# Optimization experiments

Measured on AMD Instinct MI355X. Metric: run time of the kernel, lower is better.

Reference implementation:

```python
import jax, jax.numpy as jnp
import numpy as np
from jax import lax

NUM_CLASSES = 80
RADIUS = 2.5
TOPK = 10
IOU_W = 3.0
CLS_W = 1.0
A = 33600
G = 256
IMG = 640.0


def setup_inputs() -> dict:
    key = jax.random.key(0)
    k1, k2, k3, k4, k5, k6, k7 = jax.random.split(key, 7)

    def _boxes(kc, kw, n):
        c = jax.random.uniform(kc, (n, 2), jnp.float32, 0.0, IMG)
        wh = jax.random.uniform(kw, (n, 2), jnp.float32, 8.0, 128.0)
        return jnp.concatenate([c - wh / 2, c + wh / 2], axis=1)

    return {
        "pred_scores": jax.random.normal(k1, (A, NUM_CLASSES), jnp.float32),
        "pred_bboxes": _boxes(k2, k3, A),
        "anchor_points": jax.random.uniform(k6, (A, 2), jnp.float32, 0.0, IMG),
        "gt_labels": jax.random.randint(k7, (G,), 0, NUM_CLASSES),
        "gt_bboxes": _boxes(k4, k5, G),
    }


def _inside_flags(anchor_points, gt_bboxes):
    # [G, A] bool: anchor inside GT box AND inside center-sampling region
    ax = anchor_points[None, :, 0]  # [1, A]
    ay = anchor_points[None, :, 1]
    x1, y1, x2, y2 = (gt_bboxes[:, i:i + 1] for i in range(4))  # each [G, 1]
    in_gt = (ax >= x1) & (ax <= x2) & (ay >= y1) & (ay <= y2)
    cx, cy = (x1 + x2) / 2, (y1 + y2) / 2
    rx, ry = RADIUS * (x2 - x1), RADIUS * (y2 - y1)
    in_center = (ax >= cx - rx) & (ax <= cx + rx) & (ay >= cy - ry) & (ay <= cy + ry)
    return in_gt & in_center


def _pairwise_iou(gt_bboxes, pred_bboxes, eps=1e-6):
    # [G, A]
    lt = jnp.maximum(gt_bboxes[:, None, :2], pred_bboxes[None, :, :2])
    rb = jnp.minimum(gt_bboxes[:, None, 2:], pred_bboxes[None, :, 2:])
    wh = jnp.clip(rb - lt, 0.0)
    overlap = wh[..., 0] * wh[..., 1]
    area_g = (gt_bboxes[:, 2] - gt_bboxes[:, 0]) * (gt_bboxes[:, 3] - gt_bboxes[:, 1])
    area_p = (pred_bboxes[:, 2] - pred_bboxes[:, 0]) * (pred_bboxes[:, 3] - pred_bboxes[:, 1])
    union = area_g[:, None] + area_p[None, :] - overlap + eps
    return overlap / union


def _simota(pred_scores, pred_bboxes, anchor_points, gt_labels, gt_bboxes):
    num_gt = gt_bboxes.shape[0]
    num_anchors = pred_scores.shape[0]
    gt_labels = gt_labels.astype(jnp.int32)

    inside = _inside_flags(anchor_points, gt_bboxes)  # [G, A] bool
    ious = _pairwise_iou(gt_bboxes, pred_bboxes)      # [G, A]

    # BCE(sigmoid(s), one_hot(l)) summed over classes, without [G, A, C]:
    # cost[g,a] = -sum_c log(1-p[a,c]) - (log p[a,l_g] - log(1-p[a,l_g]))
    logp = jax.nn.log_sigmoid(pred_scores)       # [A, C] = log p
    log1mp = jax.nn.log_sigmoid(-pred_scores)    # [A, C] = log(1-p)
    cls_cost = -(logp - log1mp)[:, gt_labels].T - log1mp.sum(-1)[None, :]  # [G, A]

    iou_cost = -jnp.log(ious)
    cost = CLS_W * cls_cost + IOU_W * iou_cost + (~inside).astype(cost_dtype := jnp.float32) * 1e10
    cost = lax.stop_gradient(cost)  # cost only feeds integer top-k indices

    num_candidates = ((ious * inside.astype(ious.dtype)) > 0).sum(axis=1)
    dynamic_ks = jnp.clip(num_candidates, 1, TOPK)  # [G]

    # fixed top-TOPK smallest cost per GT, mask to dynamic_k
    _, topk_idx = lax.top_k(-cost, TOPK)  # [G, TOPK]
    valid = jnp.arange(TOPK)[None, :] < dynamic_ks[:, None]
    idx = jnp.where(valid, topk_idx, num_anchors)  # invalid -> sentinel slot
    g_ids = jnp.broadcast_to(jnp.arange(num_gt, dtype=jnp.int32)[:, None], (num_gt, TOPK))
    # sequential overwrite by ascending gt index == per-anchor max gt index
    assigned = (jnp.full((num_anchors + 1,), -1, jnp.int32)
                .at[idx.reshape(-1)].max(g_ids.reshape(-1)))[:num_anchors]

    pos = assigned >= 0
    safe_g = jnp.where(pos, assigned, 0)
    assigned_labels = jnp.where(pos, gt_labels[safe_g], NUM_CLASSES)
    assigned_bboxes = jnp.where(pos[:, None], gt_bboxes[safe_g], 0.0)
    pos_iou = ious[safe_g, jnp.arange(num_anchors)]
    assigned_scores = (jnp.zeros((num_anchors, NUM_CLASSES + 1), ious.dtype)
                       .at[jnp.arange(num_anchors), assigned_labels]
                       .set(jnp.where(pos, pos_iou, 0.0)))
    return assigned_labels, assigned_bboxes, assigned_scores


def reference(pred_scores, pred_bboxes, anchor_points, gt_labels, gt_bboxes):
    return _simota(pred_scores, pred_bboxes, anchor_points, gt_labels, gt_bboxes)
```

## Files before the change

### kernel.cpp

```cpp
#include <hip/hip_runtime.h>
#include <climits>

#define A_N 33600
#define G_N 256
#define NC 80
#define KK 10
#define CAP 2048
#define NLOAD 8
#define GCHUNK 32
#define NCHUNK (G_N / GCHUNK)
#define FBSEG 16
#define FBSEG_LEN (A_N / FBSEG)
#define INIT_BLKS (A_N / 4)
#define FB_BLKS (G_N * FBSEG)

__device__ __forceinline__ unsigned int ford(float f) {
    unsigned int u = __float_as_uint(f);
    return (u & 0x80000000u) ? ~u : (u | 0x80000000u);
}

__device__ __forceinline__ unsigned long long umin64(unsigned long long a, unsigned long long b) {
    return a < b ? a : b;
}

__global__ __launch_bounds__(256) void k_init(
    const float* __restrict__ scores, const float* __restrict__ pred_b,
    const float* __restrict__ gt_b,
    float* __restrict__ logsum, int* __restrict__ cnt, int* __restrict__ assigned,
    int* __restrict__ fbseg,
    float* __restrict__ out_labels, float4* __restrict__ out_bbox4,
    float4* __restrict__ out_scores4)
{
    int b = blockIdx.x, tid = threadIdx.x;
    int lane = tid & 63, wid = tid >> 6;

    if (b >= INIT_BLKS) {
        int idx = b - INIT_BLKS;
        int g = idx >> 4, seg = idx & (FBSEG - 1);
        __shared__ int smin[4];
        float4 gb = ((const float4*)gt_b)[g];
        int best = INT_MAX;
        int a0 = seg * FBSEG_LEN;
        for (int a = a0 + tid; a < a0 + FBSEG_LEN; a += 256) {
            float4 pb = ((const float4*)pred_b)[a];
            float w = fminf(gb.z, pb.z) - fmaxf(gb.x, pb.x);
            float h = fminf(gb.w, pb.w) - fmaxf(gb.y, pb.y);
            if (w > 0.f && h > 0.f && a < best) best = a;
        }
        #pragma unroll
        for (int off = 32; off; off >>= 1) best = min(best, __shfl_down(best, off));
        if (lane == 0) smin[wid] = best;
        __syncthreads();
        if (tid == 0)
            fbseg[g * FBSEG + seg] = min(min(smin[0], smin[1]), min(smin[2], smin[3]));
        return;
    }

    int t = b * 256 + tid;
    float4 z4 = make_float4(0.f, 0.f, 0.f, 0.f);
    if (t < G_N) cnt[t] = 0;
    if (t < A_N) { assigned[t] = -1; out_labels[t] = (float)NC; out_bbox4[t] = z4; }
    if (t < (A_N * 81) / 4) out_scores4[t] = z4;

    int wv = t >> 6;
    const float* row = scores + (long)wv * NC;
    float acc = 0.f;
    for (int c = lane; c < NC; c += 64) {
        float s = row[c];
        acc -= (fmaxf(s, 0.f) + log1pf(expf(-fabsf(s))));
    }
    #pragma unroll
    for (int off = 32; off > 0; off >>= 1) acc += __shfl_down(acc, off);
    if (lane == 0) logsum[wv] = acc;
}

__global__ __launch_bounds__(256) void k_pairs(
    const float* __restrict__ scores, const float* __restrict__ pred_b,
    const float* __restrict__ anchors, const int* __restrict__ gt_labels,
    const float* __restrict__ gt_b, const float* __restrict__ logsum,
    unsigned long long* __restrict__ bucket, int* __restrict__ cnt)
{
    __shared__ float4 gbox[GCHUNK];
    __shared__ int glab[GCHUNK];
    int tid = threadIdx.x;
    int gc = blockIdx.y;
    if (tid < GCHUNK) {
        gbox[tid] = ((const float4*)gt_b)[gc * GCHUNK + tid];
        glab[tid] = gt_labels[gc * GCHUNK + tid];
    }
    __syncthreads();

    int a = blockIdx.x * 256 + tid;
    if (a >= A_N) return;

    float4 pb = ((const float4*)pred_b)[a];
    float2 ap = ((const float2*)anchors)[a];
    float area_p = (pb.z - pb.x) * (pb.w - pb.y);
    float ls = logsum[a];

    #pragma unroll 4
    for (int g = 0; g < GCHUNK; g++) {
        float4 gb = gbox[g];
        bool in_gt = (ap.x >= gb.x) & (ap.x <= gb.z) & (ap.y >= gb.y) & (ap.y <= gb.w);
        if (!in_gt) continue;

        float ltx = fmaxf(gb.x, pb.x), lty = fmaxf(gb.y, pb.y);
        float rbx = fminf(gb.z, pb.z), rby = fminf(gb.w, pb.w);
        float w = fmaxf(rbx - ltx, 0.f), h = fmaxf(rby - lty, 0.f);
        float overlap = w * h;
        if (!(overlap > 0.f)) continue;

        int gg = gc * GCHUNK + g;
        float area_g = (gb.z - gb.x) * (gb.w - gb.y);
        float uni = area_g + area_p - overlap + 1e-6f;
        float iou = overlap / uni;
        float s = scores[(long)a * NC + glab[g]];
        float cost = (-s - ls) + 3.0f * (-logf(iou));
        unsigned long long key = ((unsigned long long)ford(cost) << 32) | (unsigned)a;

        int slot = atomicAdd(&cnt[gg], 1);
        if (slot < CAP) bucket[(size_t)gg * CAP + slot] = key;
    }
}

__global__ __launch_bounds__(256) void k_select(
    const unsigned long long* __restrict__ bucket, const int* __restrict__ cnt_arr,
    const int* __restrict__ fbseg, int* __restrict__ assigned, int* __restrict__ poslist)
{
    int g = blockIdx.x, tid = threadIdx.x;
    int wid = tid >> 6, lane = tid & 63;
    __shared__ unsigned long long swin[4];
    __shared__ unsigned long long sel[KK];

    int cnt = cnt_arr[g];

    if (cnt == 0) {
        int v = (tid < FBSEG) ? fbseg[g * FBSEG + tid] : INT_MAX;
        if (tid < 64) {
            #pragma unroll
            for (int off = 8; off; off >>= 1) v = min(v, __shfl_down(v, off));
        }
        if (tid == 0) {
            if (v == INT_MAX) v = 0;
            atomicMax(&assigned[v], g);
            poslist[g * KK] = v;
            #pragma unroll
            for (int i = 1; i < KK; i++) poslist[g * KK + i] = -1;
        }
        return;
    }

    int k = cnt < KK ? cnt : KK;
    int nreal = cnt < CAP ? cnt : CAP;
    const unsigned long long* bk = bucket + (size_t)g * CAP;
    unsigned long long kv[NLOAD];
    #pragma unroll
    for (int i = 0; i < NLOAD; i++) {
        int idx = tid + i * 256;
        kv[i] = (idx < nreal) ? bk[idx] : ~0ull;
    }

    for (int it = 0; it < k; it++) {
        unsigned long long m = kv[0];
        #pragma unroll
        for (int i = 1; i < NLOAD; i++) m = umin64(m, kv[i]);
        #pragma unroll
        for (int off = 32; off; off >>= 1) m = umin64(m, __shfl_down(m, off));
        if (lane == 0) swin[wid] = m;
        __syncthreads();
        if (tid == 0)
            sel[it] = umin64(umin64(swin[0], swin[1]), umin64(swin[2], swin[3]));
        __syncthreads();
        unsigned long long win = sel[it];
        #pragma unroll
        for (int i = 0; i < NLOAD; i++) if (kv[i] == win) kv[i] = ~0ull;
    }

    if (tid < KK) poslist[g * KK + tid] = (tid < k) ? (int)(sel[tid] & 0xffffffffu) : -1;
    if (tid < k) atomicMax(&assigned[(int)(sel[tid] & 0xffffffffu)], g);
}

__global__ __launch_bounds__(256) void k_fix(
    const int* __restrict__ poslist, const int* __restrict__ assigned,
    const int* __restrict__ gt_labels, const float* __restrict__ gt_b,
    const float* __restrict__ pred_b,
    float* __restrict__ out_labels, float4* __restrict__ out_bbox4,
    float* __restrict__ out_scores)
{
    int t = blockIdx.x * 256 + threadIdx.x;
    if (t >= G_N * KK) return;
    int a = poslist[t];
    if (a < 0) return;
    int g = assigned[a];
    int label = gt_labels[g];
    float4 gb = ((const float4*)gt_b)[g];
    float4 pb = ((const float4*)pred_b)[a];
    float w = fminf(gb.z, pb.z) - fmaxf(gb.x, pb.x);
    float h = fminf(gb.w, pb.w) - fmaxf(gb.y, pb.y);
    float ovl = fmaxf(w, 0.f) * fmaxf(h, 0.f);
    float area_g = (gb.z - gb.x) * (gb.w - gb.y);
    float area_p = (pb.z - pb.x) * (pb.w - pb.y);
    float uni = area_g + area_p - ovl + 1e-6f;
    float iou = ovl / uni;
    out_labels[a] = (float)label;
    out_bbox4[a] = gb;
    out_scores[(long)a * (NC + 1) + label] = iou;
}

extern "C" void kernel_launch(void* const* d_in, const int* in_sizes, int n_in,
                              void* d_out, int out_size, void* d_ws, size_t ws_size,
                              hipStream_t stream) {
    const float* pred_scores   = (const float*)d_in[0];
    const float* pred_bboxes   = (const float*)d_in[1];
    const float* anchor_points = (const float*)d_in[2];
    const int*   gt_labels     = (const int*)d_in[3];
    const float* gt_bboxes     = (const float*)d_in[4];

    char* ws = (char*)d_ws;
    unsigned long long* bucket = (unsigned long long*)ws;
    size_t off = (size_t)G_N * CAP * 8;
    int*   assigned = (int*)(ws + off);   off += (size_t)A_N * 4;
    int*   cnt      = (int*)(ws + off);   off += (size_t)G_N * 4;
    int*   fbseg    = (int*)(ws + off);   off += (size_t)G_N * FBSEG * 4;
    int*   poslist  = (int*)(ws + off);   off += (size_t)G_N * KK * 4;
    float* logsum   = (float*)(ws + off);

    float*  out_labels = (float*)d_out;
    float4* out_bbox4  = (float4*)(out_labels + A_N);
    float*  out_scores = out_labels + 5 * (size_t)A_N;

    k_init<<<INIT_BLKS + FB_BLKS, 256, 0, stream>>>(
        pred_scores, pred_bboxes, gt_bboxes, logsum, cnt, assigned, fbseg,
        out_labels, out_bbox4, (float4*)out_scores);
    dim3 pg((A_N + 255) / 256, NCHUNK);
    k_pairs<<<pg, 256, 0, stream>>>(pred_scores, pred_bboxes, anchor_points,
                                    gt_labels, gt_bboxes, logsum, bucket, cnt);
    k_select<<<G_N, 256, 0, stream>>>(bucket, cnt, fbseg, assigned, poslist);
    k_fix<<<(G_N * KK + 255) / 256, 256, 0, stream>>>(poslist, assigned, gt_labels,
                                                      gt_bboxes, pred_bboxes,
                                                      out_labels, out_bbox4, out_scores);
}
```

Measured before the change: 45.39 us.

## Fuse init and pair kernels, recompute logsum inline, single-wave select

The init kernel and the pair-cost kernel become one launch. The BCE log-sum is computed per anchor inside each pair block, replacing the precomputed logsum buffer. The eager per-GT fallback scan over all anchors is replaced by a lazy wave-level early-exit scan inside k_select, which runs only when a GT has no candidates. k_select now uses one 64-lane wave with 32 registers per lane, so its reductions need no shared memory or block barriers, and cnt is zeroed by hipMemsetAsync. The cost is that the transcendental logsum work is repeated for each of the 8 GT chunks, and every thread reads a full strided score row.

```diff
diff --git a/kernel.cpp b/kernel.cpp
--- a/kernel.cpp
+++ b/kernel.cpp
@@ -6,13 +6,13 @@
 #define NC 80
 #define KK 10
 #define CAP 2048
-#define NLOAD 8
 #define GCHUNK 32
 #define NCHUNK (G_N / GCHUNK)
-#define FBSEG 16
-#define FBSEG_LEN (A_N / FBSEG)
-#define INIT_BLKS (A_N / 4)
-#define FB_BLKS (G_N * FBSEG)
+#define AB_N 132
+#define PAIR_BLKS (AB_N * NCHUNK)
+#define FILL_N ((A_N * 81) / 4)
+#define FILL_BLKS ((FILL_N + 255) / 256)
+#define NLD 32
 
 __device__ __forceinline__ unsigned int ford(float f) {
     unsigned int u = __float_as_uint(f);
@@ -23,80 +23,52 @@
     return a < b ? a : b;
 }
 
-__global__ __launch_bounds__(256) void k_init(
+__global__ __launch_bounds__(256) void k_main(
     const float* __restrict__ scores, const float* __restrict__ pred_b,
+    const float* __restrict__ anchors, const int* __restrict__ gt_labels,
     const float* __restrict__ gt_b,
-    float* __restrict__ logsum, int* __restrict__ cnt, int* __restrict__ assigned,
-    int* __restrict__ fbseg,
+    unsigned long long* __restrict__ bucket, int* __restrict__ cnt,
+    int* __restrict__ assigned,
     float* __restrict__ out_labels, float4* __restrict__ out_bbox4,
     float4* __restrict__ out_scores4)
 {
-    int b = blockIdx.x, tid = threadIdx.x;
-    int lane = tid & 63, wid = tid >> 6;
-
-    if (b >= INIT_BLKS) {
-        int idx = b - INIT_BLKS;
-        int g = idx >> 4, seg = idx & (FBSEG - 1);
-        __shared__ int smin[4];
-        float4 gb = ((const float4*)gt_b)[g];
-        int best = INT_MAX;
-        int a0 = seg * FBSEG_LEN;
-        for (int a = a0 + tid; a < a0 + FBSEG_LEN; a += 256) {
-            float4 pb = ((const float4*)pred_b)[a];
-            float w = fminf(gb.z, pb.z) - fmaxf(gb.x, pb.x);
-            float h = fminf(gb.w, pb.w) - fmaxf(gb.y, pb.y);
-            if (w > 0.f && h > 0.f && a < best) best = a;
-        }
-        #pragma unroll
-        for (int off = 32; off; off >>= 1) best = min(best, __shfl_down(best, off));
-        if (lane == 0) smin[wid] = best;
-        __syncthreads();
-        if (tid == 0)
-            fbseg[g * FBSEG + seg] = min(min(smin[0], smin[1]), min(smin[2], smin[3]));
+    int bid = blockIdx.x, tid = threadIdx.x;
+
+    if (bid >= PAIR_BLKS) {
+        int t = (bid - PAIR_BLKS) * 256 + tid;
+        float4 z4 = make_float4(0.f, 0.f, 0.f, 0.f);
+        if (t < A_N) { assigned[t] = -1; out_labels[t] = (float)NC; out_bbox4[t] = z4; }
+        if (t < FILL_N) out_scores4[t] = z4;
         return;
     }
 
-    int t = b * 256 + tid;
-    float4 z4 = make_float4(0.f, 0.f, 0.f, 0.f);
-    if (t < G_N) cnt[t] = 0;
-    if (t < A_N) { assigned[t] = -1; out_labels[t] = (float)NC; out_bbox4[t] = z4; }
-    if (t < (A_N * 81) / 4) out_scores4[t] = z4;
-
-    int wv = t >> 6;
-    const float* row = scores + (long)wv * NC;
-    float acc = 0.f;
-    for (int c = lane; c < NC; c += 64) {
-        float s = row[c];
-        acc -= (fmaxf(s, 0.f) + log1pf(expf(-fabsf(s))));
-    }
-    #pragma unroll
-    for (int off = 32; off > 0; off >>= 1) acc += __shfl_down(acc, off);
-    if (lane == 0) logsum[wv] = acc;
-}
-
-__global__ __launch_bounds__(256) void k_pairs(
-    const float* __restrict__ scores, const float* __restrict__ pred_b,
-    const float* __restrict__ anchors, const int* __restrict__ gt_labels,
-    const float* __restrict__ gt_b, const float* __restrict__ logsum,
-    unsigned long long* __restrict__ bucket, int* __restrict__ cnt)
-{
     __shared__ float4 gbox[GCHUNK];
     __shared__ int glab[GCHUNK];
-    int tid = threadIdx.x;
-    int gc = blockIdx.y;
+    int gc = bid & (NCHUNK - 1);
+    int ab = bid >> 3;
     if (tid < GCHUNK) {
         gbox[tid] = ((const float4*)gt_b)[gc * GCHUNK + tid];
         glab[tid] = gt_labels[gc * GCHUNK + tid];
     }
     __syncthreads();
 
-    int a = blockIdx.x * 256 + tid;
+    int a = ab * 256 + tid;
     if (a >= A_N) return;
 
     float4 pb = ((const float4*)pred_b)[a];
     float2 ap = ((const float2*)anchors)[a];
     float area_p = (pb.z - pb.x) * (pb.w - pb.y);
-    float ls = logsum[a];
+
+    const float4* row = (const float4*)(scores + (long)a * NC);
+    float ls = 0.f;
+    #pragma unroll 4
+    for (int i = 0; i < NC / 4; i++) {
+        float4 v = row[i];
+        ls -= fmaxf(v.x, 0.f) + log1pf(expf(-fabsf(v.x)));
+        ls -= fmaxf(v.y, 0.f) + log1pf(expf(-fabsf(v.y)));
+        ls -= fmaxf(v.z, 0.f) + log1pf(expf(-fabsf(v.z)));
+        ls -= fmaxf(v.w, 0.f) + log1pf(expf(-fabsf(v.w)));
+    }
 
     #pragma unroll 4
     for (int g = 0; g < GCHUNK; g++) {
@@ -119,65 +91,65 @@
         unsigned long long key = ((unsigned long long)ford(cost) << 32) | (unsigned)a;
 
         int slot = atomicAdd(&cnt[gg], 1);
-        if (slot < CAP) bucket[(size_t)gg * CAP + slot] = key;
-    }
-}
-
-__global__ __launch_bounds__(256) void k_select(
+        if ((unsigned)slot < CAP) bucket[(size_t)gg * CAP + slot] = key;
+    }
+}
+
+__global__ __launch_bounds__(64) void k_select(
     const unsigned long long* __restrict__ bucket, const int* __restrict__ cnt_arr,
-    const int* __restrict__ fbseg, int* __restrict__ assigned, int* __restrict__ poslist)
+    const float* __restrict__ pred_b, const float* __restrict__ gt_b,
+    int* __restrict__ assigned, int* __restrict__ poslist)
 {
-    int g = blockIdx.x, tid = threadIdx.x;
-    int wid = tid >> 6, lane = tid & 63;
-    __shared__ unsigned long long swin[4];
-    __shared__ unsigned long long sel[KK];
-
+    int g = blockIdx.x, lane = threadIdx.x;
     int cnt = cnt_arr[g];
 
     if (cnt == 0) {
-        int v = (tid < FBSEG) ? fbseg[g * FBSEG + tid] : INT_MAX;
-        if (tid < 64) {
-            #pragma unroll
-            for (int off = 8; off; off >>= 1) v = min(v, __shfl_down(v, off));
+        float4 gb = ((const float4*)gt_b)[g];
+        int found = INT_MAX;
+        for (int base = 0; base < A_N; base += 64) {
+            int a = base + lane;
+            float4 pb = ((const float4*)pred_b)[a];
+            float w = fminf(gb.z, pb.z) - fmaxf(gb.x, pb.x);
+            float h = fminf(gb.w, pb.w) - fmaxf(gb.y, pb.y);
+            bool hit = (w > 0.f) && (h > 0.f);
+            if (__ballot(hit)) { if (hit) found = a; break; }
         }
-        if (tid == 0) {
-            if (v == INT_MAX) v = 0;
-            atomicMax(&assigned[v], g);
-            poslist[g * KK] = v;
-            #pragma unroll
-            for (int i = 1; i < KK; i++) poslist[g * KK + i] = -1;
-        }
+        #pragma unroll
+        for (int off = 32; off; off >>= 1) found = min(found, __shfl_xor(found, off));
+        int m = (found == INT_MAX) ? 0 : found;
+        if (lane == 0) atomicMax(&assigned[m], g);
+        if (lane < KK) poslist[g * KK + lane] = (lane == 0) ? m : -1;
         return;
     }
 
     int k = cnt < KK ? cnt : KK;
     int nreal = cnt < CAP ? cnt : CAP;
     const unsigned long long* bk = bucket + (size_t)g * CAP;
-    unsigned long long kv[NLOAD];
+
+    unsigned long long kv[NLD];
     #pragma unroll
-    for (int i = 0; i < NLOAD; i++) {
-        int idx = tid + i * 256;
-        kv[i] = (idx < nreal) ? bk[idx] : ~0ull;
-    }
-
+    for (int i = 0; i < NLD; i++) {
+        kv[i] = ~0ull;
+        if (i * 64 < nreal) {
+            int idx = lane + i * 64;
+            if (idx < nreal) kv[i] = bk[idx];
+        }
+    }
+
+    int mywin = -1;
     for (int it = 0; it < k; it++) {
-        unsigned long long m = kv[0];
-        #pragma unroll
-        for (int i = 1; i < NLOAD; i++) m = umin64(m, kv[i]);
-        #pragma unroll
-        for (int off = 32; off; off >>= 1) m = umin64(m, __shfl_down(m, off));
-        if (lane == 0) swin[wid] = m;
-        __syncthreads();
-        if (tid == 0)
-            sel[it] = umin64(umin64(swin[0], swin[1]), umin64(swin[2], swin[3]));
-        __syncthreads();
-        unsigned long long win = sel[it];
-        #pragma unroll
-        for (int i = 0; i < NLOAD; i++) if (kv[i] == win) kv[i] = ~0ull;
-    }
-
-    if (tid < KK) poslist[g * KK + tid] = (tid < k) ? (int)(sel[tid] & 0xffffffffu) : -1;
-    if (tid < k) atomicMax(&assigned[(int)(sel[tid] & 0xffffffffu)], g);
+        unsigned long long m = ~0ull;
+        #pragma unroll
+        for (int i = 0; i < NLD; i++) if (i * 64 < nreal) m = umin64(m, kv[i]);
+        #pragma unroll
+        for (int off = 32; off; off >>= 1) m = umin64(m, __shfl_xor(m, off));
+        if (lane == it) mywin = (int)(m & 0xffffffffu);
+        #pragma unroll
+        for (int i = 0; i < NLD; i++) if (i * 64 < nreal) { if (kv[i] == m) kv[i] = ~0ull; }
+    }
+
+    if (lane < KK) poslist[g * KK + lane] = (lane < k) ? mywin : -1;
+    if (lane < k) atomicMax(&assigned[mywin], g);
 }
 
 __global__ __launch_bounds__(256) void k_fix(
@@ -219,23 +191,20 @@
     char* ws = (char*)d_ws;
     unsigned long long* bucket = (unsigned long long*)ws;
     size_t off = (size_t)G_N * CAP * 8;
-    int*   assigned = (int*)(ws + off);   off += (size_t)A_N * 4;
-    int*   cnt      = (int*)(ws + off);   off += (size_t)G_N * 4;
-    int*   fbseg    = (int*)(ws + off);   off += (size_t)G_N * FBSEG * 4;
-    int*   poslist  = (int*)(ws + off);   off += (size_t)G_N * KK * 4;
-    float* logsum   = (float*)(ws + off);
+    int* assigned = (int*)(ws + off);   off += (size_t)A_N * 4;
+    int* cnt      = (int*)(ws + off);   off += (size_t)G_N * 4;
+    int* poslist  = (int*)(ws + off);
 
     float*  out_labels = (float*)d_out;
     float4* out_bbox4  = (float4*)(out_labels + A_N);
     float*  out_scores = out_labels + 5 * (size_t)A_N;
 
-    k_init<<<INIT_BLKS + FB_BLKS, 256, 0, stream>>>(
-        pred_scores, pred_bboxes, gt_bboxes, logsum, cnt, assigned, fbseg,
-        out_labels, out_bbox4, (float4*)out_scores);
-    dim3 pg((A_N + 255) / 256, NCHUNK);
-    k_pairs<<<pg, 256, 0, stream>>>(pred_scores, pred_bboxes, anchor_points,
-                                    gt_labels, gt_bboxes, logsum, bucket, cnt);
-    k_select<<<G_N, 256, 0, stream>>>(bucket, cnt, fbseg, assigned, poslist);
+    hipMemsetAsync(cnt, 0, (size_t)G_N * sizeof(int), stream);
+    k_main<<<PAIR_BLKS + FILL_BLKS, 256, 0, stream>>>(
+        pred_scores, pred_bboxes, anchor_points, gt_labels, gt_bboxes,
+        bucket, cnt, assigned, out_labels, out_bbox4, (float4*)out_scores);
+    k_select<<<G_N, 64, 0, stream>>>(bucket, cnt, pred_bboxes, gt_bboxes,
+                                     assigned, poslist);
     k_fix<<<(G_N * KK + 255) / 256, 256, 0, stream>>>(poslist, assigned, gt_labels,
                                                       gt_bboxes, pred_bboxes,
                                                       out_labels, out_bbox4, out_scores);
```

Result: slower. 110.5 us (+143.4%).
